# Performance work log

Measured on AMD Instinct MI355X. Metric: run time of the kernel, lower is better.

Reference implementation:

```python
import jax, jax.numpy as jnp
import numpy as np

N = 50000   # num_nodes in batch
E = 200000  # num_possible_edges_in_batch
H = 768     # config.hidden_size (BERT cls dim)
D1 = 256    # args.gnn_layer1_out_dim
C = 2       # num_classes
EDGE_PERCENT = 0.1


def setup_inputs() -> dict:
    key = jax.random.key(0)
    ks = jax.random.split(key, 6)
    x = jax.random.normal(ks[0], (N, H), jnp.float32)
    edge_src = jax.random.randint(ks[1], (E,), 0, N, dtype=jnp.int32)
    edge_dst = jax.random.randint(ks[2], (E,), 0, N, dtype=jnp.int32)
    labels = jax.random.randint(ks[3], (E,), 0, C, dtype=jnp.int32)
    # xavier-uniform-ish init scale
    W1 = jax.random.normal(ks[4], (D1, 2 * H), jnp.float32) / np.sqrt(2 * H).astype(np.float32)
    b1 = jnp.zeros((D1,), jnp.float32)
    W2 = jax.random.normal(ks[5], (C, D1), jnp.float32) / np.sqrt(D1).astype(np.float32)
    b2 = jnp.zeros((C,), jnp.float32)
    class_weights = jnp.array([EDGE_PERCENT, 1.0 - EDGE_PERCENT], jnp.float32)
    return {"x": x, "W1": W1, "b1": b1, "W2": W2, "b2": b2,
            "class_weights": class_weights,
            "edge_src": edge_src, "edge_dst": edge_dst, "labels": labels}


def reference(x, W1, b1, W2, b2, class_weights, edge_src, edge_dst, labels):
    # Per-edge gather + concat of endpoint node embeddings: [E, 2H]
    edge_repr = jnp.concatenate([x[edge_src], x[edge_dst]], axis=-1)
    # linear1 -> gelu (torch default = exact erf gelu) -> linear2
    h = jax.nn.gelu(edge_repr @ W1.T + b1, approximate=False)   # [E, D1]
    logits = h @ W2.T + b2                                       # [E, C]
    probs = jax.nn.softmax(logits, axis=-1)
    # weighted CrossEntropyLoss (torch semantics: sum(w_y * nll) / sum(w_y))
    logp = jax.nn.log_softmax(logits, axis=-1)
    nll = -jnp.take_along_axis(logp, labels[:, None].astype(jnp.int32), axis=1)[:, 0]
    w = class_weights[labels]
    loss = jnp.sum(w * nll) / jnp.sum(w)
    return loss, probs
```

## Files before the change

### kernel.cpp

```cpp
#include <hip/hip_runtime.h>
#include <math.h>
#include <stdint.h>

#define NN 50000
#define NE 200000
#define HD 768
#define TWOH 1536
#define DD1 256
#define NOUT 512
#define BM 128
#define BK 64
#define KST 12
#define KSTEPS 24

#define NB_CVT 9375
#define NB_SWZ 192

#define EPB 10
#define EBLK (EPB * 32)

typedef __bf16 bf16_t;
typedef _Float16 f16_t;
typedef __attribute__((ext_vector_type(8))) __bf16 bf16x8;
typedef __attribute__((ext_vector_type(8))) _Float16 f16x8;
typedef __attribute__((ext_vector_type(4))) _Float16 f16x4;
typedef __attribute__((ext_vector_type(4))) float f32x4;

__device__ __forceinline__ void gl2lds16(const void* g, void* l) {
    __builtin_amdgcn_global_load_lds(
        (const __attribute__((address_space(1))) unsigned int*)g,
        (__attribute__((address_space(3))) unsigned int*)l,
        16, 0, 0);
}

__device__ __forceinline__ float gelu_erf(float v) {
    float xa = fabsf(v) * 0.70710678118654752f;
    float t  = __builtin_amdgcn_rcpf(fmaf(0.3275911f, xa, 1.0f));
    float pl = fmaf(fmaf(fmaf(fmaf(1.061405429f, t, -1.453152027f), t,
                   1.421413741f), t, -0.284496736f), t, 0.254829592f) * t;
    float er = fmaf(-pl, __expf(-xa * xa), 1.0f);
    er = copysignf(er, v);
    return 0.5f * v * (1.0f + er);
}

__global__ void prep_all(const float* __restrict__ x, bf16_t* __restrict__ xb,
                         const float* __restrict__ w1, bf16_t* __restrict__ w1s,
                         const float* __restrict__ b1, const float* __restrict__ w2,
                         float* __restrict__ pw)
{
    const int b = blockIdx.x;
    const int t = threadIdx.x;
    if (b < NB_CVT) {
        const int i = b * 256 + t;
        const float4* p = (const float4*)x + (size_t)i * 4;
        float4 a = p[0], bq = p[1], c = p[2], d = p[3];
        bf16x8 o0, o1;
        o0[0]=(bf16_t)a.x; o0[1]=(bf16_t)a.y; o0[2]=(bf16_t)a.z; o0[3]=(bf16_t)a.w;
        o0[4]=(bf16_t)bq.x; o0[5]=(bf16_t)bq.y; o0[6]=(bf16_t)bq.z; o0[7]=(bf16_t)bq.w;
        o1[0]=(bf16_t)c.x; o1[1]=(bf16_t)c.y; o1[2]=(bf16_t)c.z; o1[3]=(bf16_t)c.w;
        o1[4]=(bf16_t)d.x; o1[5]=(bf16_t)d.y; o1[6]=(bf16_t)d.z; o1[7]=(bf16_t)d.w;
        bf16x8* q = (bf16x8*)(xb + (size_t)i * 16);
        q[0] = o0; q[1] = o1;
    } else if (b < NB_CVT + NB_SWZ) {
        const int idx = (b - NB_CVT) * 256 + t;
        const int n  = idx & 255;
        const int kc = (idx >> 8) & 7;
        const int ks = idx >> 11;
        const float* gp = w1 + (size_t)n * TWOH + ks * BK + kc * 8;
        float4 v0 = ((const float4*)gp)[0];
        float4 v1 = ((const float4*)gp)[1];
        bf16x8 o;
        o[0]=(bf16_t)v0.x; o[1]=(bf16_t)v0.y; o[2]=(bf16_t)v0.z; o[3]=(bf16_t)v0.w;
        o[4]=(bf16_t)v1.x; o[5]=(bf16_t)v1.y; o[6]=(bf16_t)v1.z; o[7]=(bf16_t)v1.w;
        *(bf16x8*)(w1s + (size_t)idx * 8) = o;
    } else {
        const int s = t;
        const int k = s & 63;
        const int c = (s & 192) + ((k & 3) << 4) + (k >> 2);
        pw[s]       = b1[c];
        pw[256 + s] = w2[c];
        pw[512 + s] = w2[DD1 + c];
    }
}

__global__ void finalize_kernel(float* __restrict__ out, const float* __restrict__ accum) {
    out[0] = accum[0] / accum[1];
}

__global__ __launch_bounds__(512, 4)
void node_gemm3(const bf16_t* __restrict__ xb, const bf16_t* __restrict__ w1s,
                f16_t* __restrict__ h)
{
    __shared__ __align__(16) char smem[65536];

    const int t = threadIdx.x;
    const int lane = t & 63;
    const int wv = t >> 6;
    const int wm = wv & 1;
    const int wn = wv >> 1;
    const int q = lane >> 4;
    const int r = lane & 15;

    const int nwg = 391 * 2;
    const int qq = nwg >> 3, rr8 = nwg & 7;
    int bid = blockIdx.x;
    int xcd = bid & 7, ii = bid >> 3;
    int wg = (xcd < rr8 ? xcd * (qq + 1) : rr8 * (qq + 1) + (xcd - rr8) * qq) + ii;
    const int mtile = wg >> 1;
    const int nb2 = wg & 1;

    const int r0 = t >> 3;
    const int gsl = (t & 7) ^ (r0 & 7);
    int row0 = mtile * BM + r0;        if (row0 >= NN) row0 = NN - 1;
    int row1 = mtile * BM + 64 + r0;   if (row1 >= NN) row1 = NN - 1;
    const bf16_t* gA0 = xb + (size_t)row0 * HD + gsl * 8;
    const bf16_t* gA1 = xb + (size_t)row1 * HD + gsl * 8;

    auto stageA = [&](int ks, char* Ab) {
        gl2lds16(gA0 + ks * BK, (bf16_t*)Ab + t * 8);
        gl2lds16(gA1 + ks * BK, (bf16_t*)Ab + 4096 + t * 8);
    };

    f32x4 acc[4][4];
    #pragma unroll
    for (int a_ = 0; a_ < 4; ++a_)
        #pragma unroll
        for (int b_ = 0; b_ < 4; ++b_) acc[a_][b_] = (f32x4){0.f, 0.f, 0.f, 0.f};

    const bf16_t* w1base = w1s + (size_t)nb2 * KST * 16384;

    stageA(0, smem);

    for (int ks = 0; ks < KST; ++ks) {
        bf16_t* Ac = (bf16_t*)(smem + ((ks & 1) << 14));
        char*   An = smem + ((~ks & 1) << 14);
        bf16_t* Bl = (bf16_t*)(smem + 32768);

        __syncthreads();

        #pragma unroll
        for (int i = 0; i < 4; ++i) {
            const int ci = i * 512 + t;
            gl2lds16(w1base + (size_t)ks * 16384 + (size_t)ci * 8, Bl + ci * 8);
        }
        const bool pf = (ks + 1 < KST);
        if (pf) stageA(ks + 1, An);

        if (pf) asm volatile("s_waitcnt vmcnt(2)\n\ts_barrier" ::: "memory");
        else    asm volatile("s_waitcnt vmcnt(0)\n\ts_barrier" ::: "memory");

        #pragma unroll
        for (int kk = 0; kk < 2; ++kk) {
            bf16x8 af[4];
            const int sl = (kk * 4 + q) ^ (r & 7);
            #pragma unroll
            for (int mb = 0; mb < 4; ++mb)
                af[mb] = *(const bf16x8*)(Ac + (wm * 64 + mb * 16 + r) * 64 + sl * 8);
            #pragma unroll
            for (int nb = 0; nb < 4; ++nb) {
                bf16x8 bfr = *(const bf16x8*)(Bl + (size_t)(((kk * 4 + q) << 8) + wn * 64 + nb * 16 + r) * 8);
                #pragma unroll
                for (int mb = 0; mb < 4; ++mb)
                    acc[mb][nb] = __builtin_amdgcn_mfma_f32_16x16x32_bf16(af[mb], bfr, acc[mb][nb], 0, 0, 0);
            }
        }
    }

    #pragma unroll
    for (int mb = 0; mb < 4; ++mb) {
        #pragma unroll
        for (int rr = 0; rr < 4; ++rr) {
            const int grow = mtile * BM + wm * 64 + mb * 16 + q * 4 + rr;
            if (grow < NN) {
                f16x4 o;
                #pragma unroll
                for (int nb = 0; nb < 4; ++nb) o[nb] = (f16_t)acc[mb][nb][rr];
                *(f16x4*)(h + (size_t)grow * NOUT + nb2 * DD1 + wn * 64 + r * 4) = o;
            }
        }
    }
}

__device__ __forceinline__ void edge_compute(
    f16x8 a0, f16x8 a1, f16x8 a2, f16x8 a3,
    f16x8 c0v, f16x8 c1v, f16x8 c2v, f16x8 c3v,
    int e, int lb, int p, const float* lds_pw,
    float b20, float b21, float cw0, float cw1,
    float* __restrict__ out, float& wnll_t, float& wsum_t)
{
    float l0 = 0.f, l1 = 0.f;
#define GRP(ha, hb, g) { \
        const int c0_ = (g) * 64 + p * 8; \
        float4 ba = *(const float4*)(&lds_pw[c0_]); \
        float4 bb = *(const float4*)(&lds_pw[c0_ + 4]); \
        float4 wa = *(const float4*)(&lds_pw[256 + c0_]); \
        float4 wb = *(const float4*)(&lds_pw[256 + c0_ + 4]); \
        float4 va = *(const float4*)(&lds_pw[512 + c0_]); \
        float4 vb = *(const float4*)(&lds_pw[512 + c0_ + 4]); \
        float gl; \
        gl = gelu_erf((float)ha[0] + (float)hb[0] + ba.x); l0 = fmaf(gl, wa.x, l0); l1 = fmaf(gl, va.x, l1); \
        gl = gelu_erf((float)ha[1] + (float)hb[1] + ba.y); l0 = fmaf(gl, wa.y, l0); l1 = fmaf(gl, va.y, l1); \
        gl = gelu_erf((float)ha[2] + (float)hb[2] + ba.z); l0 = fmaf(gl, wa.z, l0); l1 = fmaf(gl, va.z, l1); \
        gl = gelu_erf((float)ha[3] + (float)hb[3] + ba.w); l0 = fmaf(gl, wa.w, l0); l1 = fmaf(gl, va.w, l1); \
        gl = gelu_erf((float)ha[4] + (float)hb[4] + bb.x); l0 = fmaf(gl, wb.x, l0); l1 = fmaf(gl, vb.x, l1); \
        gl = gelu_erf((float)ha[5] + (float)hb[5] + bb.y); l0 = fmaf(gl, wb.y, l0); l1 = fmaf(gl, vb.y, l1); \
        gl = gelu_erf((float)ha[6] + (float)hb[6] + bb.z); l0 = fmaf(gl, wb.z, l0); l1 = fmaf(gl, vb.z, l1); \
        gl = gelu_erf((float)ha[7] + (float)hb[7] + bb.w); l0 = fmaf(gl, wb.w, l0); l1 = fmaf(gl, vb.w, l1); \
    }
    GRP(a0, c0v, 0)
    GRP(a1, c1v, 1)
    GRP(a2, c2v, 2)
    GRP(a3, c3v, 3)
#undef GRP
    l0 += __shfl_xor(l0, 1); l0 += __shfl_xor(l0, 2); l0 += __shfl_xor(l0, 4);
    l1 += __shfl_xor(l1, 1); l1 += __shfl_xor(l1, 2); l1 += __shfl_xor(l1, 4);
    if (p == 0) {
        float L0 = l0 + b20, L1 = l1 + b21;
        float mx = fmaxf(L0, L1);
        float ex0 = __expf(L0 - mx), ex1 = __expf(L1 - mx);
        float s = ex0 + ex1, inv = 1.f / s;
        out[1 + 2 * e] = ex0 * inv;
        out[2 + 2 * e] = ex1 * inv;
        float w = lb ? cw1 : cw0;
        wnll_t += w * (mx + logf(s) - (lb ? L1 : L0));
        wsum_t += w;
    }
}

__global__ __launch_bounds__(256, 4)
void edge_mlp6(const f16_t* __restrict__ h, const float* __restrict__ pw,
               const float* __restrict__ b2, const float* __restrict__ cw,
               const int* __restrict__ esrc, const int* __restrict__ edst,
               const int* __restrict__ lab, float* __restrict__ out,
               float* __restrict__ accum)
{
    __shared__ float lds_pw[768];
    __shared__ float red[8];
    const int t = threadIdx.x;
    const int lane = t & 63;
    const int wv = t >> 6;
    const int slot = t >> 3;
    const int p = t & 7;

    for (int i = t; i < 768; i += 256) lds_pw[i] = pw[i];

    const float b20 = b2[0], b21 = b2[1];
    const float cw0 = cw[0], cw1 = cw[1];
    const int e0i = blockIdx.x * EBLK + slot;

    float wnll_t = 0.f, wsum_t = 0.f;

    int Xe, Xs, Xd, Xlb, Ye, Ys, Yd, Ylb;
    f16x8 Xa0, Xa1, Xa2, Xa3, Xc0, Xc1, Xc2, Xc3;
    f16x8 Ya0, Ya1, Ya2, Ya3, Yc0, Yc1, Yc2, Yc3;

#define META(B, k) { B##e = e0i + (k) * 32; B##s = esrc[B##e]; B##d = edst[B##e]; B##lb = lab[B##e]; }
#define DATA(B) { \
        const f16_t* sp_ = h + (size_t)B##s * NOUT + p * 8; \
        const f16_t* dp_ = h + (size_t)B##d * NOUT + DD1 + p * 8; \
        B##a0 = *(const f16x8*)(sp_);        B##a1 = *(const f16x8*)(sp_ + 64); \
        B##a2 = *(const f16x8*)(sp_ + 128);  B##a3 = *(const f16x8*)(sp_ + 192); \
        B##c0 = *(const f16x8*)(dp_);        B##c1 = *(const f16x8*)(dp_ + 64); \
        B##c2 = *(const f16x8*)(dp_ + 128);  B##c3 = *(const f16x8*)(dp_ + 192); }

    META(X, 0)
    DATA(X)
    META(Y, 1)
    __syncthreads();

    for (int k = 0; k < EPB; k += 2) {
        DATA(Y)
        {
            const int eC = Xe, lbC = Xlb;
            if (k + 2 < EPB) META(X, k + 2)
            edge_compute(Xa0, Xa1, Xa2, Xa3, Xc0, Xc1, Xc2, Xc3,
                         eC, lbC, p, lds_pw, b20, b21, cw0, cw1, out, wnll_t, wsum_t);
        }
        __builtin_amdgcn_sched_barrier(0);
        if (k + 2 < EPB) DATA(X)
        {
            const int eC = Ye, lbC = Ylb;
            if (k + 3 < EPB) META(Y, k + 3)
            edge_compute(Ya0, Ya1, Ya2, Ya3, Yc0, Yc1, Yc2, Yc3,
                         eC, lbC, p, lds_pw, b20, b21, cw0, cw1, out, wnll_t, wsum_t);
        }
        __builtin_amdgcn_sched_barrier(0);
    }
#undef META
#undef DATA

    wnll_t += __shfl_xor(wnll_t, 8);  wsum_t += __shfl_xor(wsum_t, 8);
    wnll_t += __shfl_xor(wnll_t, 16); wsum_t += __shfl_xor(wsum_t, 16);
    wnll_t += __shfl_xor(wnll_t, 32); wsum_t += __shfl_xor(wsum_t, 32);
    if (lane == 0) { red[wv] = wnll_t; red[4 + wv] = wsum_t; }
    __syncthreads();
    if (t == 0) {
        float a_ = red[0] + red[1] + red[2] + red[3];
        float b_ = red[4] + red[5] + red[6] + red[7];
        atomicAdd(&accum[0], a_);
        atomicAdd(&accum[1], b_);
    }
}

template<bool XPRE, bool WPRE>
__global__ __launch_bounds__(512, 4)
void fused_edge_mlp(const float* __restrict__ xf, const bf16_t* __restrict__ xb,
                    const float* __restrict__ w1f, const bf16_t* __restrict__ w1s,
                    const float* __restrict__ b1, const float* __restrict__ w2,
                    const float* __restrict__ b2, const float* __restrict__ cw,
                    const int* __restrict__ esrc, const int* __restrict__ edst,
                    const int* __restrict__ lab, float* __restrict__ out,
                    float* __restrict__ accum)
{
    __shared__ __align__(16) char smem[65536];
    const int t = threadIdx.x;
    const int lane = t & 63;
    const int wv = t >> 6;
    const int wm = wv & 1;
    const int wn = wv >> 1;
    const int q = lane >> 4;
    const int r = lane & 15;
    const int ebase = blockIdx.x * BM;
    const int r0 = t >> 3;
    const int e1c = (ebase + r0 + 64 < NE) ? (ebase + r0 + 64) : 0;
    const int ns0 = esrc[ebase + r0];
    const int nd0 = edst[ebase + r0];
    const int ns1 = esrc[e1c];
    const int nd1 = edst[e1c];
    const int gsl = (t & 7) ^ (r0 & 7);

    f32x4 acc[4][4];
    #pragma unroll
    for (int a_ = 0; a_ < 4; ++a_)
        #pragma unroll
        for (int b_ = 0; b_ < 4; ++b_) acc[a_][b_] = (f32x4){0.f, 0.f, 0.f, 0.f};

    auto stageA = [&](int kp, char* AbBase) {
        const bool issrc = (kp < 12);
        const int col0 = issrc ? kp * BK : kp * BK - HD;
        #pragma unroll
        for (int i = 0; i < 2; ++i) {
            const int node = i ? (issrc ? ns1 : nd1) : (issrc ? ns0 : nd0);
            bf16_t* lp = (bf16_t*)AbBase + i * 4096 + t * 8;
            if (XPRE) {
                gl2lds16(xb + (size_t)node * HD + col0 + gsl * 8, lp);
            } else {
                const float* gp = xf + (size_t)node * HD + col0 + gsl * 8;
                float4 v0 = ((const float4*)gp)[0];
                float4 v1 = ((const float4*)gp)[1];
                bf16x8 o;
                o[0]=(bf16_t)v0.x; o[1]=(bf16_t)v0.y; o[2]=(bf16_t)v0.z; o[3]=(bf16_t)v0.w;
                o[4]=(bf16_t)v1.x; o[5]=(bf16_t)v1.y; o[6]=(bf16_t)v1.z; o[7]=(bf16_t)v1.w;
                *(bf16x8*)lp = o;
            }
        }
    };

    stageA(0, smem);

    for (int ks = 0; ks < KSTEPS; ++ks) {
        bf16_t* Ac = (bf16_t*)(smem + ((ks & 1) << 14));
        char*   An = smem + ((~ks & 1) << 14);
        bf16_t* Bl = (bf16_t*)(smem + 32768);
        __syncthreads();
        #pragma unroll
        for (int i = 0; i < 4; ++i) {
            const int ci = i * 512 + t;
            bf16_t* lp = Bl + ci * 8;
            if (WPRE) {
                gl2lds16(w1s + (size_t)ks * 16384 + ci * 8, lp);
            } else {
                const int n = ci & 255, kc = ci >> 8;
                const float* gp = w1f + (size_t)n * TWOH + ks * BK + kc * 8;
                float4 v0 = ((const float4*)gp)[0];
                float4 v1 = ((const float4*)gp)[1];
                bf16x8 o;
                o[0]=(bf16_t)v0.x; o[1]=(bf16_t)v0.y; o[2]=(bf16_t)v0.z; o[3]=(bf16_t)v0.w;
                o[4]=(bf16_t)v1.x; o[5]=(bf16_t)v1.y; o[6]=(bf16_t)v1.z; o[7]=(bf16_t)v1.w;
                *(bf16x8*)lp = o;
            }
        }
        if (XPRE && WPRE)
            asm volatile("s_waitcnt vmcnt(0)\n\ts_barrier" ::: "memory");
        else
            __syncthreads();
        if (ks + 1 < KSTEPS) stageA(ks + 1, An);
        #pragma unroll
        for (int kk = 0; kk < 2; ++kk) {
            bf16x8 af[4];
            const int sl = (kk * 4 + q) ^ (r & 7);
            #pragma unroll
            for (int mb = 0; mb < 4; ++mb) {
                const int m = wm * 64 + mb * 16 + r;
                af[mb] = *(const bf16x8*)(Ac + m * 64 + sl * 8);
            }
            #pragma unroll
            for (int nb = 0; nb < 4; ++nb) {
                bf16x8 bfr = *(const bf16x8*)(Bl + (size_t)(((kk * 4 + q) << 8) + wn * 64 + nb * 16 + r) * 8);
                #pragma unroll
                for (int mb = 0; mb < 4; ++mb)
                    acc[mb][nb] = __builtin_amdgcn_mfma_f32_16x16x32_bf16(af[mb], bfr, acc[mb][nb], 0, 0, 0);
            }
        }
    }

    bf16_t* Hl = (bf16_t*)smem;
    float* red = (float*)(smem + 32768);
    float bias[4];
    #pragma unroll
    for (int nb = 0; nb < 4; ++nb) bias[nb] = b1[wn * 64 + nb * 16 + r];

    float wnll_t = 0.f, wsum_t = 0.f;
    const int ml2 = t >> 3;
    const int p = t & 7;

    #pragma unroll
    for (int half = 0; half < 2; ++half) {
        __syncthreads();
        if (wm == half) {
            #pragma unroll
            for (int mb = 0; mb < 4; ++mb)
                #pragma unroll
                for (int nb = 0; nb < 4; ++nb)
                    #pragma unroll
                    for (int rr = 0; rr < 4; ++rr) {
                        int ml = mb * 16 + q * 4 + rr;
                        int col = wn * 64 + nb * 16 + r;
                        float v = acc[mb][nb][rr] + bias[nb];
                        float g = 0.5f * v * (1.f + erff(v * 0.70710678118654752f));
                        int swcol = ((((col >> 3) ^ (ml & 7)) << 3) | (col & 7));
                        Hl[ml * 256 + swcol] = (bf16_t)g;
                    }
        }
        __syncthreads();
        float l0 = 0.f, l1 = 0.f;
        #pragma unroll
        for (int j = 0; j < 4; ++j) {
            int cj = p * 4 + j;
            bf16x8 hv = *(const bf16x8*)(Hl + ml2 * 256 + ((cj ^ (ml2 & 7)) << 3));
            const float4* w2a = (const float4*)(w2 + cj * 8);
            const float4* w2b = (const float4*)(w2 + 256 + cj * 8);
            float4 wa0 = w2a[0], wa1 = w2a[1], wb0 = w2b[0], wb1 = w2b[1];
            float hf[8];
            #pragma unroll
            for (int u = 0; u < 8; ++u) hf[u] = (float)hv[u];
            l0 += hf[0]*wa0.x + hf[1]*wa0.y + hf[2]*wa0.z + hf[3]*wa0.w
                + hf[4]*wa1.x + hf[5]*wa1.y + hf[6]*wa1.z + hf[7]*wa1.w;
            l1 += hf[0]*wb0.x + hf[1]*wb0.y + hf[2]*wb0.z + hf[3]*wb0.w
                + hf[4]*wb1.x + hf[5]*wb1.y + hf[6]*wb1.z + hf[7]*wb1.w;
        }
        l0 += __shfl_xor(l0, 1); l0 += __shfl_xor(l0, 2); l0 += __shfl_xor(l0, 4);
        l1 += __shfl_xor(l1, 1); l1 += __shfl_xor(l1, 2); l1 += __shfl_xor(l1, 4);
        const int eg = ebase + half * 64 + ml2;
        if (p == 0 && eg < NE) {
            l0 += b2[0]; l1 += b2[1];
            float mx = fmaxf(l0, l1);
            float e0 = expf(l0 - mx), e1 = expf(l1 - mx);
            float s = e0 + e1;
            float inv = 1.f / s;
            out[1 + 2 * eg] = e0 * inv;
            out[2 + 2 * eg] = e1 * inv;
            int lb = lab[eg];
            float w = cw[lb];
            float lpv = ((lb ? l1 : l0) - mx) - logf(s);
            wnll_t -= w * lpv;
            wsum_t += w;
        }
    }
    #pragma unroll
    for (int o = 1; o < 64; o <<= 1) {
        wnll_t += __shfl_xor(wnll_t, o);
        wsum_t += __shfl_xor(wsum_t, o);
    }
    __syncthreads();
    if (lane == 0) { red[wv] = wnll_t; red[8 + wv] = wsum_t; }
    __syncthreads();
    if (t == 0) {
        float a_ = 0.f, b_ = 0.f;
        #pragma unroll
        for (int i = 0; i < 8; ++i) { a_ += red[i]; b_ += red[8 + i]; }
        atomicAdd(&accum[0], a_);
        atomicAdd(&accum[1], b_);
    }
}

extern "C" void kernel_launch(void* const* d_in, const int* in_sizes, int n_in,
                              void* d_out, int out_size, void* d_ws, size_t ws_size,
                              hipStream_t stream)
{
    (void)in_sizes; (void)n_in; (void)out_size;
    const float* x  = (const float*)d_in[0];
    const float* W1 = (const float*)d_in[1];
    const float* b1 = (const float*)d_in[2];
    const float* W2 = (const float*)d_in[3];
    const float* b2 = (const float*)d_in[4];
    const float* cw = (const float*)d_in[5];
    const int* esrc = (const int*)d_in[6];
    const int* edst = (const int*)d_in[7];
    const int* lab  = (const int*)d_in[8];
    float* out = (float*)d_out;
    char* ws = (char*)d_ws;

    float* accum = (float*)ws;
    const size_t off_w1 = 256;
    const size_t w1s_bytes = (size_t)DD1 * TWOH * 2;
    const size_t off_pw = off_w1 + w1s_bytes;
    const size_t off_h  = off_pw + 3072;
    const size_t h_bytes = (size_t)NN * NOUT * 2;
    const size_t off_xb = off_h + h_bytes;
    const size_t xb_bytes = (size_t)NN * HD * 2;
    const size_t off_xb2 = off_h;

    (void)hipMemsetAsync(accum, 0, 2 * sizeof(float), stream);

    if (ws_size >= off_xb + xb_bytes) {
        bf16_t* w1s = (bf16_t*)(ws + off_w1);
        float* pw = (float*)(ws + off_pw);
        f16_t* h = (f16_t*)(ws + off_h);
        bf16_t* xb = (bf16_t*)(ws + off_xb);
        prep_all<<<NB_CVT + NB_SWZ + 1, 256, 0, stream>>>(x, xb, W1, w1s, b1, W2, pw);
        node_gemm3<<<391 * 2, 512, 0, stream>>>(xb, w1s, h);
        edge_mlp6<<<NE / EBLK, 256, 0, stream>>>(h, pw, b2, cw, esrc, edst, lab, out, accum);
    } else if (ws_size >= off_xb2 + xb_bytes) {
        bf16_t* w1s = (bf16_t*)(ws + off_w1);
        float* pw = (float*)(ws + off_pw);
        bf16_t* xb = (bf16_t*)(ws + off_xb2);
        prep_all<<<NB_CVT + NB_SWZ + 1, 256, 0, stream>>>(x, xb, W1, w1s, b1, W2, pw);
        dim3 grid((NE + BM - 1) / BM);
        fused_edge_mlp<true, true><<<grid, 512, 0, stream>>>(
            x, xb, W1, w1s, b1, W2, b2, cw, esrc, edst, lab, out, accum);
    } else {
        dim3 grid((NE + BM - 1) / BM);
        fused_edge_mlp<false, false><<<grid, 512, 0, stream>>>(
            x, (const bf16_t*)ws, W1, (const bf16_t*)ws, b1, W2, b2, cw,
            esrc, edst, lab, out, accum);
    }

    finalize_kernel<<<1, 1, 0, stream>>>(out, accum);
}
```

Measured before the change: 336.3 us.

## Fuse x fp32-to-bf16 conversion into node GEMM A-tile loading

Removes the separate pass that converted all node features to bf16 in the workspace. The node GEMM now loads fp32 x rows into registers, converts them, and writes swizzled bf16 into a single LDS buffer, prefetching the next K-step through registers. This removes a full write and re-read of the bf16 copy and a large launch. In exchange, fp32 x is read by both column-half tiles and the async LDS double buffer is lost. The fallback paths are simplified accordingly.

```diff
diff --git a/kernel.cpp b/kernel.cpp
--- a/kernel.cpp
+++ b/kernel.cpp
@@ -13,7 +13,6 @@
 #define KST 12
 #define KSTEPS 24
 
-#define NB_CVT 9375
 #define NB_SWZ 192
 
 #define EPB 10
@@ -43,26 +42,14 @@
     return 0.5f * v * (1.0f + er);
 }
 
-__global__ void prep_all(const float* __restrict__ x, bf16_t* __restrict__ xb,
-                         const float* __restrict__ w1, bf16_t* __restrict__ w1s,
-                         const float* __restrict__ b1, const float* __restrict__ w2,
-                         float* __restrict__ pw)
+__global__ void prep_w(const float* __restrict__ w1, bf16_t* __restrict__ w1s,
+                       const float* __restrict__ b1, const float* __restrict__ w2,
+                       float* __restrict__ pw)
 {
     const int b = blockIdx.x;
     const int t = threadIdx.x;
-    if (b < NB_CVT) {
-        const int i = b * 256 + t;
-        const float4* p = (const float4*)x + (size_t)i * 4;
-        float4 a = p[0], bq = p[1], c = p[2], d = p[3];
-        bf16x8 o0, o1;
-        o0[0]=(bf16_t)a.x; o0[1]=(bf16_t)a.y; o0[2]=(bf16_t)a.z; o0[3]=(bf16_t)a.w;
-        o0[4]=(bf16_t)bq.x; o0[5]=(bf16_t)bq.y; o0[6]=(bf16_t)bq.z; o0[7]=(bf16_t)bq.w;
-        o1[0]=(bf16_t)c.x; o1[1]=(bf16_t)c.y; o1[2]=(bf16_t)c.z; o1[3]=(bf16_t)c.w;
-        o1[4]=(bf16_t)d.x; o1[5]=(bf16_t)d.y; o1[6]=(bf16_t)d.z; o1[7]=(bf16_t)d.w;
-        bf16x8* q = (bf16x8*)(xb + (size_t)i * 16);
-        q[0] = o0; q[1] = o1;
-    } else if (b < NB_CVT + NB_SWZ) {
-        const int idx = (b - NB_CVT) * 256 + t;
+    if (b < NB_SWZ) {
+        const int idx = b * 256 + t;
         const int n  = idx & 255;
         const int kc = (idx >> 8) & 7;
         const int ks = idx >> 11;
@@ -88,10 +75,10 @@
 }
 
 __global__ __launch_bounds__(512, 4)
-void node_gemm3(const bf16_t* __restrict__ xb, const bf16_t* __restrict__ w1s,
+void node_gemm5(const float* __restrict__ x, const bf16_t* __restrict__ w1s,
                 f16_t* __restrict__ h)
 {
-    __shared__ __align__(16) char smem[65536];
+    __shared__ __align__(16) char smem[49152];
 
     const int t = threadIdx.x;
     const int lane = t & 63;
@@ -109,16 +96,29 @@
     const int mtile = wg >> 1;
     const int nb2 = wg & 1;
 
-    const int r0 = t >> 3;
-    const int gsl = (t & 7) ^ (r0 & 7);
-    int row0 = mtile * BM + r0;        if (row0 >= NN) row0 = NN - 1;
-    int row1 = mtile * BM + 64 + r0;   if (row1 >= NN) row1 = NN - 1;
-    const bf16_t* gA0 = xb + (size_t)row0 * HD + gsl * 8;
-    const bf16_t* gA1 = xb + (size_t)row1 * HD + gsl * 8;
-
-    auto stageA = [&](int ks, char* Ab) {
-        gl2lds16(gA0 + ks * BK, (bf16_t*)Ab + t * 8);
-        gl2lds16(gA1 + ks * BK, (bf16_t*)Ab + 4096 + t * 8);
+    const int arow = t >> 2;
+    const int achk = t & 3;
+    int grow = mtile * BM + arow;  if (grow >= NN) grow = NN - 1;
+    const float* gA = x + (size_t)grow * HD + achk * 16;
+
+    bf16_t* Al = (bf16_t*)smem;
+    bf16_t* Bl = (bf16_t*)(smem + 16384);
+
+    float4 pr[4];
+    auto loadA = [&](int ks) {
+        const float4* p = (const float4*)(gA + ks * BK);
+        pr[0] = p[0]; pr[1] = p[1]; pr[2] = p[2]; pr[3] = p[3];
+    };
+    auto writeA = [&]() {
+        bf16x8 o0, o1;
+        o0[0]=(bf16_t)pr[0].x; o0[1]=(bf16_t)pr[0].y; o0[2]=(bf16_t)pr[0].z; o0[3]=(bf16_t)pr[0].w;
+        o0[4]=(bf16_t)pr[1].x; o0[5]=(bf16_t)pr[1].y; o0[6]=(bf16_t)pr[1].z; o0[7]=(bf16_t)pr[1].w;
+        o1[0]=(bf16_t)pr[2].x; o1[1]=(bf16_t)pr[2].y; o1[2]=(bf16_t)pr[2].z; o1[3]=(bf16_t)pr[2].w;
+        o1[4]=(bf16_t)pr[3].x; o1[5]=(bf16_t)pr[3].y; o1[6]=(bf16_t)pr[3].z; o1[7]=(bf16_t)pr[3].w;
+        const int c0 = achk * 2;
+        bf16_t* base = Al + arow * 64;
+        *(bf16x8*)(base + ((c0 ^ (arow & 7)) << 3))       = o0;
+        *(bf16x8*)(base + (((c0 + 1) ^ (arow & 7)) << 3)) = o1;
     };
 
     f32x4 acc[4][4];
@@ -129,13 +129,9 @@
 
     const bf16_t* w1base = w1s + (size_t)nb2 * KST * 16384;
 
-    stageA(0, smem);
+    loadA(0);
 
     for (int ks = 0; ks < KST; ++ks) {
-        bf16_t* Ac = (bf16_t*)(smem + ((ks & 1) << 14));
-        char*   An = smem + ((~ks & 1) << 14);
-        bf16_t* Bl = (bf16_t*)(smem + 32768);
-
         __syncthreads();
 
         #pragma unroll
@@ -143,11 +139,10 @@
             const int ci = i * 512 + t;
             gl2lds16(w1base + (size_t)ks * 16384 + (size_t)ci * 8, Bl + ci * 8);
         }
-        const bool pf = (ks + 1 < KST);
-        if (pf) stageA(ks + 1, An);
-
-        if (pf) asm volatile("s_waitcnt vmcnt(2)\n\ts_barrier" ::: "memory");
-        else    asm volatile("s_waitcnt vmcnt(0)\n\ts_barrier" ::: "memory");
+        writeA();
+        if (ks + 1 < KST) loadA(ks + 1);
+
+        __syncthreads();
 
         #pragma unroll
         for (int kk = 0; kk < 2; ++kk) {
@@ -155,7 +150,7 @@
             const int sl = (kk * 4 + q) ^ (r & 7);
             #pragma unroll
             for (int mb = 0; mb < 4; ++mb)
-                af[mb] = *(const bf16x8*)(Ac + (wm * 64 + mb * 16 + r) * 64 + sl * 8);
+                af[mb] = *(const bf16x8*)(Al + (wm * 64 + mb * 16 + r) * 64 + sl * 8);
             #pragma unroll
             for (int nb = 0; nb < 4; ++nb) {
                 bf16x8 bfr = *(const bf16x8*)(Bl + (size_t)(((kk * 4 + q) << 8) + wn * 64 + nb * 16 + r) * 8);
@@ -170,12 +165,12 @@
     for (int mb = 0; mb < 4; ++mb) {
         #pragma unroll
         for (int rr = 0; rr < 4; ++rr) {
-            const int grow = mtile * BM + wm * 64 + mb * 16 + q * 4 + rr;
-            if (grow < NN) {
+            const int gr2 = mtile * BM + wm * 64 + mb * 16 + q * 4 + rr;
+            if (gr2 < NN) {
                 f16x4 o;
                 #pragma unroll
                 for (int nb = 0; nb < 4; ++nb) o[nb] = (f16_t)acc[mb][nb][rr];
-                *(f16x4*)(h + (size_t)grow * NOUT + nb2 * DD1 + wn * 64 + r * 4) = o;
+                *(f16x4*)(h + (size_t)gr2 * NOUT + nb2 * DD1 + wn * 64 + r * 4) = o;
             }
         }
     }
@@ -302,10 +297,8 @@
     }
 }
 
-template<bool XPRE, bool WPRE>
 __global__ __launch_bounds__(512, 4)
-void fused_edge_mlp(const float* __restrict__ xf, const bf16_t* __restrict__ xb,
-                    const float* __restrict__ w1f, const bf16_t* __restrict__ w1s,
+void fused_fallback(const float* __restrict__ xf, const float* __restrict__ w1f,
                     const float* __restrict__ b1, const float* __restrict__ w2,
                     const float* __restrict__ b2, const float* __restrict__ cw,
                     const int* __restrict__ esrc, const int* __restrict__ edst,
@@ -342,17 +335,13 @@
         for (int i = 0; i < 2; ++i) {
             const int node = i ? (issrc ? ns1 : nd1) : (issrc ? ns0 : nd0);
             bf16_t* lp = (bf16_t*)AbBase + i * 4096 + t * 8;
-            if (XPRE) {
-                gl2lds16(xb + (size_t)node * HD + col0 + gsl * 8, lp);
-            } else {
-                const float* gp = xf + (size_t)node * HD + col0 + gsl * 8;
-                float4 v0 = ((const float4*)gp)[0];
-                float4 v1 = ((const float4*)gp)[1];
-                bf16x8 o;
-                o[0]=(bf16_t)v0.x; o[1]=(bf16_t)v0.y; o[2]=(bf16_t)v0.z; o[3]=(bf16_t)v0.w;
-                o[4]=(bf16_t)v1.x; o[5]=(bf16_t)v1.y; o[6]=(bf16_t)v1.z; o[7]=(bf16_t)v1.w;
-                *(bf16x8*)lp = o;
-            }
+            const float* gp = xf + (size_t)node * HD + col0 + gsl * 8;
+            float4 v0 = ((const float4*)gp)[0];
+            float4 v1 = ((const float4*)gp)[1];
+            bf16x8 o;
+            o[0]=(bf16_t)v0.x; o[1]=(bf16_t)v0.y; o[2]=(bf16_t)v0.z; o[3]=(bf16_t)v0.w;
+            o[4]=(bf16_t)v1.x; o[5]=(bf16_t)v1.y; o[6]=(bf16_t)v1.z; o[7]=(bf16_t)v1.w;
+            *(bf16x8*)lp = o;
         }
     };
 
@@ -367,23 +356,16 @@
         for (int i = 0; i < 4; ++i) {
             const int ci = i * 512 + t;
             bf16_t* lp = Bl + ci * 8;
-            if (WPRE) {
-                gl2lds16(w1s + (size_t)ks * 16384 + ci * 8, lp);
-            } else {
-                const int n = ci & 255, kc = ci >> 8;
-                const float* gp = w1f + (size_t)n * TWOH + ks * BK + kc * 8;
-                float4 v0 = ((const float4*)gp)[0];
-                float4 v1 = ((const float4*)gp)[1];
-                bf16x8 o;
-                o[0]=(bf16_t)v0.x; o[1]=(bf16_t)v0.y; o[2]=(bf16_t)v0.z; o[3]=(bf16_t)v0.w;
-                o[4]=(bf16_t)v1.x; o[5]=(bf16_t)v1.y; o[6]=(bf16_t)v1.z; o[7]=(bf16_t)v1.w;
-                *(bf16x8*)lp = o;
-            }
-        }
-        if (XPRE && WPRE)
-            asm volatile("s_waitcnt vmcnt(0)\n\ts_barrier" ::: "memory");
-        else
-            __syncthreads();
+            const int n = ci & 255, kc = ci >> 8;
+            const float* gp = w1f + (size_t)n * TWOH + ks * BK + kc * 8;
+            float4 v0 = ((const float4*)gp)[0];
+            float4 v1 = ((const float4*)gp)[1];
+            bf16x8 o;
+            o[0]=(bf16_t)v0.x; o[1]=(bf16_t)v0.y; o[2]=(bf16_t)v0.z; o[3]=(bf16_t)v0.w;
+            o[4]=(bf16_t)v1.x; o[5]=(bf16_t)v1.y; o[6]=(bf16_t)v1.z; o[7]=(bf16_t)v1.w;
+            *(bf16x8*)lp = o;
+        }
+        __syncthreads();
         if (ks + 1 < KSTEPS) stageA(ks + 1, An);
         #pragma unroll
         for (int kk = 0; kk < 2; ++kk) {
@@ -507,33 +489,20 @@
     const size_t off_pw = off_w1 + w1s_bytes;
     const size_t off_h  = off_pw + 3072;
     const size_t h_bytes = (size_t)NN * NOUT * 2;
-    const size_t off_xb = off_h + h_bytes;
-    const size_t xb_bytes = (size_t)NN * HD * 2;
-    const size_t off_xb2 = off_h;
 
     (void)hipMemsetAsync(accum, 0, 2 * sizeof(float), stream);
 
-    if (ws_size >= off_xb + xb_bytes) {
+    if (ws_size >= off_h + h_bytes) {
         bf16_t* w1s = (bf16_t*)(ws + off_w1);
         float* pw = (float*)(ws + off_pw);
         f16_t* h = (f16_t*)(ws + off_h);
-        bf16_t* xb = (bf16_t*)(ws + off_xb);
-        prep_all<<<NB_CVT + NB_SWZ + 1, 256, 0, stream>>>(x, xb, W1, w1s, b1, W2, pw);
-        node_gemm3<<<391 * 2, 512, 0, stream>>>(xb, w1s, h);
+        prep_w<<<NB_SWZ + 1, 256, 0, stream>>>(W1, w1s, b1, W2, pw);
+        node_gemm5<<<391 * 2, 512, 0, stream>>>(x, w1s, h);
         edge_mlp6<<<NE / EBLK, 256, 0, stream>>>(h, pw, b2, cw, esrc, edst, lab, out, accum);
-    } else if (ws_size >= off_xb2 + xb_bytes) {
-        bf16_t* w1s = (bf16_t*)(ws + off_w1);
-        float* pw = (float*)(ws + off_pw);
-        bf16_t* xb = (bf16_t*)(ws + off_xb2);
-        prep_all<<<NB_CVT + NB_SWZ + 1, 256, 0, stream>>>(x, xb, W1, w1s, b1, W2, pw);
-        dim3 grid((NE + BM - 1) / BM);
-        fused_edge_mlp<true, true><<<grid, 512, 0, stream>>>(
-            x, xb, W1, w1s, b1, W2, b2, cw, esrc, edst, lab, out, accum);
     } else {
         dim3 grid((NE + BM - 1) / BM);
-        fused_edge_mlp<false, false><<<grid, 512, 0, stream>>>(
-            x, (const bf16_t*)ws, W1, (const bf16_t*)ws, b1, W2, b2, cw,
-            esrc, edst, lab, out, accum);
+        fused_fallback<<<grid, 512, 0, stream>>>(
+            x, W1, b1, W2, b2, cw, esrc, edst, lab, out, accum);
     }
 
     finalize_kernel<<<1, 1, 0, stream>>>(out, accum);
```

New measurement: 333.5 us. About the same (-0.9%).
